# Kernel tuning notes

Measured on AMD Instinct MI355X. Metric: run time of the kernel, lower is better.

The kernel has to match this reference:

```python
import jax, jax.numpy as jnp
import numpy as np

TEMP = 0.07


def setup_inputs() -> dict:
    key = jax.random.key(0)
    k1, k2 = jax.random.split(key)
    N, C = 8192, 512
    X = jax.random.normal(k1, (N, C), dtype=jnp.float32)
    Y = jax.random.normal(k2, (N, C), dtype=jnp.float32)
    return {"X": X, "Y": Y}


def reference(X, Y):
    # Original loop computes, per row i, cross-entropy over logits
    # [X_i.Y_i, X_i.Y_j (j != i)] / temp with label 0 (the positive).
    # Softmax CE is permutation-invariant, so this equals
    #   logsumexp(S_i / temp) - S_ii / temp,  S = X @ Y^T,
    # summed over rows (loop accumulates with +=, i.e. sum reduction).
    S = jnp.einsum('nc,mc->nm', X, Y) / TEMP  # [N, N]
    lse = jax.nn.logsumexp(S, axis=1)          # [N]
    pos = jnp.diagonal(S)                      # [N]
    return jnp.sum(lse - pos)
```

## Files before the change

kernel.cpp:

```cpp
#include <hip/hip_runtime.h>
#include <stdint.h>

#define N 8192
#define C 512
#define BM 256
#define BN 128
#define BKF 128
#define NSPLIT 8
#define COLS_PER_SPLIT (N / NSPLIT)
#define CT (COLS_PER_SPLIT / BN)
#define GRID_GEMM ((N / BM) * NSPLIT)
#define INV_T 14.285714285714286f

typedef __attribute__((ext_vector_type(4)))  int   i32x4;
typedef __attribute__((ext_vector_type(8)))  int   i32x8;
typedef __attribute__((ext_vector_type(16))) float f32x16;

__global__ __launch_bounds__(256) void prep_kernel(const float* __restrict__ X,
                                                   const float* __restrict__ Y,
                                                   unsigned char* __restrict__ Xf8,
                                                   unsigned char* __restrict__ Yf8,
                                                   float* __restrict__ pos,
                                                   int* __restrict__ cnt,
                                                   float* __restrict__ out) {
  if (blockIdx.x == 0) {
    if (threadIdx.x < (N / BM)) cnt[threadIdx.x] = 0;
    if (threadIdx.x == 64) *out = 0.0f;
  }
  const int wave = threadIdx.x >> 6;
  const int lane = threadIdx.x & 63;
  const int row = blockIdx.x * 4 + wave;
  const float4* xr = (const float4*)(X + (size_t)row * C) + lane * 2;
  const float4* yr = (const float4*)(Y + (size_t)row * C) + lane * 2;
  float4 x0 = xr[0], x1 = xr[1];
  float4 y0 = yr[0], y1 = yr[1];
  float s = x0.x * y0.x + x0.y * y0.y + x0.z * y0.z + x0.w * y0.w
          + x1.x * y1.x + x1.y * y1.y + x1.z * y1.z + x1.w * y1.w;
  int2 ox, oy;
  ox.x = __builtin_amdgcn_cvt_pk_fp8_f32(x0.x, x0.y, 0, false);
  ox.x = __builtin_amdgcn_cvt_pk_fp8_f32(x0.z, x0.w, ox.x, true);
  ox.y = __builtin_amdgcn_cvt_pk_fp8_f32(x1.x, x1.y, 0, false);
  ox.y = __builtin_amdgcn_cvt_pk_fp8_f32(x1.z, x1.w, ox.y, true);
  oy.x = __builtin_amdgcn_cvt_pk_fp8_f32(y0.x, y0.y, 0, false);
  oy.x = __builtin_amdgcn_cvt_pk_fp8_f32(y0.z, y0.w, oy.x, true);
  oy.y = __builtin_amdgcn_cvt_pk_fp8_f32(y1.x, y1.y, 0, false);
  oy.y = __builtin_amdgcn_cvt_pk_fp8_f32(y1.z, y1.w, oy.y, true);
  ((int2*)(Xf8 + (size_t)row * C))[lane] = ox;
  ((int2*)(Yf8 + (size_t)row * C))[lane] = oy;
#pragma unroll
  for (int off = 32; off >= 1; off >>= 1) s += __shfl_xor(s, off);
  if (lane == 0) pos[row] = s * INV_T;
}

__global__ __launch_bounds__(256, 1) void gemm_lse_kernel(const unsigned char* __restrict__ Xf8,
                                                          const unsigned char* __restrict__ Yf8,
                                                          float2* __restrict__ partials,
                                                          const float* __restrict__ pos,
                                                          int* __restrict__ cnt,
                                                          float* __restrict__ out) {
  __shared__ unsigned char Bs[2][BN][BKF];
  __shared__ float wsum[4];
  __shared__ int mflag;

  const int tid = threadIdx.x;
  const int bx = blockIdx.x;
  const int split = bx & (NSPLIT - 1);
  const int rb = bx >> 3;
  const int row0 = rb * BM;
  const int colbase = split * COLS_PER_SPLIT;

  const int w = tid >> 6;
  const int lane = tid & 63;
  const int lrow = lane & 31;
  const int h = lane >> 5;
  const int swz = lrow & 7;

  i32x4 tL0[8], tH0[8], tL1[8], tH1[8];
  {
    const unsigned char* a0 = Xf8 + (size_t)(row0 + w * 64 + lrow) * C + h * 32;
    const unsigned char* a1 = a0 + (size_t)32 * C;
#pragma unroll
    for (int kk = 0; kk < 8; ++kk) {
      asm volatile("global_load_dwordx4 %0, %1, off"
                   : "=v"(tL0[kk]) : "v"(a0 + kk * 64));
      asm volatile("global_load_dwordx4 %0, %1, off offset:16"
                   : "=v"(tH0[kk]) : "v"(a0 + kk * 64));
      asm volatile("global_load_dwordx4 %0, %1, off"
                   : "=v"(tL1[kk]) : "v"(a1 + kk * 64));
      asm volatile("global_load_dwordx4 %0, %1, off offset:16"
                   : "=v"(tH1[kk]) : "v"(a1 + kk * 64));
    }
  }

  const int r_base = tid >> 3;
  const int p = tid & 7;
  const int j = p ^ (r_base & 7);

  auto stageB = [&](int buf, int col0, int k0) {
#pragma unroll
    for (int i = 0; i < 4; ++i) {
      const int r = i * 32 + r_base;
      const unsigned char* gb = Yf8 + (size_t)(col0 + r) * C + k0 * BKF + j * 16;
      uint32_t loff = (uint32_t)((i * 256 + (tid & ~63)) * 16);
      __builtin_amdgcn_global_load_lds(
          (const __attribute__((address_space(1))) uint32_t*)(uintptr_t)gb,
          (__attribute__((address_space(3))) uint32_t*)(uintptr_t)((char*)&Bs[buf][0][0] + loff),
          16, 0, 0);
    }
  };

  stageB(0, colbase, 0);
  asm volatile("s_waitcnt vmcnt(0)" ::: "memory");
  __builtin_amdgcn_sched_barrier(0);
  __builtin_amdgcn_s_barrier();
  __builtin_amdgcn_sched_barrier(0);

  i32x8 aF0[8], aF1[8];
#pragma unroll
  for (int kk = 0; kk < 8; ++kk) {
    aF0[kk] = (i32x8){ tL0[kk][0], tL0[kk][1], tL0[kk][2], tL0[kk][3],
                       tH0[kk][0], tH0[kk][1], tH0[kk][2], tH0[kk][3] };
    aF1[kk] = (i32x8){ tL1[kk][0], tL1[kk][1], tL1[kk][2], tL1[kk][3],
                       tH1[kk][0], tH1[kk][1], tH1[kk][2], tH1[kk][3] };
  }

  float m0[16], l0[16], m1[16], l1[16];
#pragma unroll
  for (int s = 0; s < 16; ++s) {
    m0[s] = -INFINITY; l0[s] = 0.0f;
    m1[s] = -INFINITY; l1[s] = 0.0f;
  }

  for (int ct = 0; ct < CT; ++ct) {
    f32x16 acc0[4], acc1[4];
#pragma unroll
    for (int t = 0; t < 4; ++t)
#pragma unroll
      for (int e = 0; e < 16; ++e) { acc0[t][e] = 0.0f; acc1[t][e] = 0.0f; }

#pragma unroll
    for (int k0 = 0; k0 < 4; ++k0) {
      const int nct = (k0 == 3) ? ((ct + 1) & (CT - 1)) : ct;
      const int nk0 = (k0 + 1) & 3;
      stageB((k0 + 1) & 1, colbase + nct * BN, nk0);
      __builtin_amdgcn_sched_barrier(0);
      asm volatile("s_waitcnt vmcnt(4)" ::: "memory");
      __builtin_amdgcn_s_barrier();
      __builtin_amdgcn_sched_barrier(0);

      __builtin_amdgcn_s_setprio(1);
#pragma unroll
      for (int s = 0; s < 2; ++s) {
        const int kk = 2 * k0 + s;
        const int c0 = 4 * s + 2 * h;
#pragma unroll
        for (int tj = 0; tj < 4; ++tj) {
          const int brow = tj * 32 + lrow;
          i32x4 blo = *(const i32x4*)&Bs[k0 & 1][brow][((c0    ) ^ swz) * 16];
          i32x4 bhi = *(const i32x4*)&Bs[k0 & 1][brow][((c0 + 1) ^ swz) * 16];
          i32x8 bf = { blo[0], blo[1], blo[2], blo[3], bhi[0], bhi[1], bhi[2], bhi[3] };
          acc0[tj] = __builtin_amdgcn_mfma_scale_f32_32x32x64_f8f6f4(
              aF0[kk], bf, acc0[tj], 0, 0, 0, 127, 0, 127);
          acc1[tj] = __builtin_amdgcn_mfma_scale_f32_32x32x64_f8f6f4(
              aF1[kk], bf, acc1[tj], 0, 0, 0, 127, 0, 127);
        }
      }
      __builtin_amdgcn_s_setprio(0);
      __builtin_amdgcn_sched_barrier(0);
      __builtin_amdgcn_s_barrier();
      __builtin_amdgcn_sched_barrier(0);
    }

#pragma unroll
    for (int r = 0; r < 16; ++r) {
      {
        float v0 = acc0[0][r] * INV_T, v1 = acc0[1][r] * INV_T;
        float v2 = acc0[2][r] * INV_T, v3 = acc0[3][r] * INV_T;
        float mx = fmaxf(fmaxf(v0, v1), fmaxf(v2, v3));
        float mn = fmaxf(m0[r], mx);
        l0[r] = l0[r] * __expf(m0[r] - mn)
              + __expf(v0 - mn) + __expf(v1 - mn) + __expf(v2 - mn) + __expf(v3 - mn);
        m0[r] = mn;
      }
      {
        float v0 = acc1[0][r] * INV_T, v1 = acc1[1][r] * INV_T;
        float v2 = acc1[2][r] * INV_T, v3 = acc1[3][r] * INV_T;
        float mx = fmaxf(fmaxf(v0, v1), fmaxf(v2, v3));
        float mn = fmaxf(m1[r], mx);
        l1[r] = l1[r] * __expf(m1[r] - mn)
              + __expf(v0 - mn) + __expf(v1 - mn) + __expf(v2 - mn) + __expf(v3 - mn);
        m1[r] = mn;
      }
    }
  }

  asm volatile("s_waitcnt vmcnt(0)" ::: "memory");

#pragma unroll
  for (int r = 0; r < 16; ++r) {
    float ma = m0[r], la = l0[r], mb = m1[r], lb = l1[r];
#pragma unroll
    for (int off = 1; off < 32; off <<= 1) {
      float mo = __shfl_xor(ma, off), lo = __shfl_xor(la, off);
      float mn = fmaxf(ma, mo);
      la = la * __expf(ma - mn) + lo * __expf(mo - mn);
      ma = mn;
      float mo2 = __shfl_xor(mb, off), lo2 = __shfl_xor(lb, off);
      float mn2 = fmaxf(mb, mo2);
      lb = lb * __expf(mb - mn2) + lo2 * __expf(mo2 - mn2);
      mb = mn2;
    }
    m0[r] = ma; l0[r] = la; m1[r] = mb; l1[r] = lb;
  }
  if (lrow == 0) {
#pragma unroll
    for (int r = 0; r < 16; ++r) {
      int row_local = (r & 3) + 8 * (r >> 2) + 4 * h;
      int base = row0 + w * 64;
      partials[(size_t)split * N + (base + row_local)]      = make_float2(m0[r], l0[r]);
      partials[(size_t)split * N + (base + 32 + row_local)] = make_float2(m1[r], l1[r]);
    }
  }

  __syncthreads();
  if (tid == 0) {
    __threadfence();
    int old = atomicAdd(&cnt[rb], 1);
    mflag = (old == NSPLIT - 1) ? 1 : 0;
  }
  __syncthreads();
  if (mflag) {
    __threadfence();
    int row = row0 + tid;
    float M = -INFINITY, L = 0.0f;
#pragma unroll
    for (int s = 0; s < NSPLIT; ++s) {
      float2 pr = partials[(size_t)s * N + row];
      float mn = fmaxf(M, pr.x);
      L = L * __expf(M - mn) + pr.y * __expf(pr.x - mn);
      M = mn;
    }
    float v = M + __logf(L) - pos[row];
#pragma unroll
    for (int off = 32; off >= 1; off >>= 1) v += __shfl_xor(v, off);
    if (lane == 0) wsum[w] = v;
    __syncthreads();
    if (tid == 0) atomicAdd(out, wsum[0] + wsum[1] + wsum[2] + wsum[3]);
  }
}

extern "C" void kernel_launch(void* const* d_in, const int* in_sizes, int n_in,
                              void* d_out, int out_size, void* d_ws, size_t ws_size,
                              hipStream_t stream) {
  const float* X = (const float*)d_in[0];
  const float* Y = (const float*)d_in[1];
  float* out = (float*)d_out;

  char* w = (char*)d_ws;
  unsigned char* Xf8 = (unsigned char*)w;
  unsigned char* Yf8 = Xf8 + (size_t)N * C;
  float2* partials = (float2*)(Yf8 + (size_t)N * C);
  float* pos = (float*)((char*)partials + (size_t)NSPLIT * N * sizeof(float2));
  int* cnt = (int*)(pos + N);

  prep_kernel<<<N / 4, 256, 0, stream>>>(X, Y, Xf8, Yf8, pos, cnt, out);
  gemm_lse_kernel<<<GRID_GEMM, 256, 0, stream>>>(Xf8, Yf8, partials, pos, cnt, out);
}
```

Measured before the change: 140.2 us.

## Shrink row tile to 64, split columns across waves, use exp2 online softmax

Reduces the GEMM row tile from 256 to 64 rows so each wave handles a 32-column slice of the B tile instead of all 128 columns. This quadruples the grid and allows two blocks per CU, targeting occupancy and per-wave register pressure. The cost is less A/B reuse per block: each staged B tile now feeds only 64 rows, so B traffic rises fourfold. The LSE update switches to base-2 exponentials with a prescaled factor, and a shared-memory cross-wave merge is added before partials are written.

```diff
diff --git a/kernel.cpp b/kernel.cpp
--- a/kernel.cpp
+++ b/kernel.cpp
@@ -3,14 +3,17 @@
 
 #define N 8192
 #define C 512
-#define BM 256
+#define BM 64
 #define BN 128
 #define BKF 128
 #define NSPLIT 8
 #define COLS_PER_SPLIT (N / NSPLIT)
 #define CT (COLS_PER_SPLIT / BN)
-#define GRID_GEMM ((N / BM) * NSPLIT)
+#define NRB (N / BM)
+#define GRID_GEMM (NRB * NSPLIT)
 #define INV_T 14.285714285714286f
+#define SCALE2 20.60992915555662f
+#define LN2F 0.6931471805599453f
 
 typedef __attribute__((ext_vector_type(4)))  int   i32x4;
 typedef __attribute__((ext_vector_type(8)))  int   i32x8;
@@ -24,8 +27,8 @@
                                                    int* __restrict__ cnt,
                                                    float* __restrict__ out) {
   if (blockIdx.x == 0) {
-    if (threadIdx.x < (N / BM)) cnt[threadIdx.x] = 0;
-    if (threadIdx.x == 64) *out = 0.0f;
+    if (threadIdx.x < NRB) cnt[threadIdx.x] = 0;
+    if (threadIdx.x == 128) *out = 0.0f;
   }
   const int wave = threadIdx.x >> 6;
   const int lane = threadIdx.x & 63;
@@ -52,7 +55,7 @@
   if (lane == 0) pos[row] = s * INV_T;
 }
 
-__global__ __launch_bounds__(256, 1) void gemm_lse_kernel(const unsigned char* __restrict__ Xf8,
+__global__ __launch_bounds__(256, 2) void gemm_lse_kernel(const unsigned char* __restrict__ Xf8,
                                                           const unsigned char* __restrict__ Yf8,
                                                           float2* __restrict__ partials,
                                                           const float* __restrict__ pos,
@@ -74,21 +77,15 @@
   const int lrow = lane & 31;
   const int h = lane >> 5;
   const int swz = lrow & 7;
-
-  i32x4 tL0[8], tH0[8], tL1[8], tH1[8];
+  const int brow = w * 32 + lrow;
+
+  i32x8 aF0[8], aF1[8];
   {
-    const unsigned char* a0 = Xf8 + (size_t)(row0 + w * 64 + lrow) * C + h * 32;
-    const unsigned char* a1 = a0 + (size_t)32 * C;
+    const unsigned char* a0 = Xf8 + (size_t)(row0 + lrow) * C + h * 32;
 #pragma unroll
     for (int kk = 0; kk < 8; ++kk) {
-      asm volatile("global_load_dwordx4 %0, %1, off"
-                   : "=v"(tL0[kk]) : "v"(a0 + kk * 64));
-      asm volatile("global_load_dwordx4 %0, %1, off offset:16"
-                   : "=v"(tH0[kk]) : "v"(a0 + kk * 64));
-      asm volatile("global_load_dwordx4 %0, %1, off"
-                   : "=v"(tL1[kk]) : "v"(a1 + kk * 64));
-      asm volatile("global_load_dwordx4 %0, %1, off offset:16"
-                   : "=v"(tH1[kk]) : "v"(a1 + kk * 64));
+      aF0[kk] = *(const i32x8*)(a0 + kk * 64);
+      aF1[kk] = *(const i32x8*)(a0 + (size_t)32 * C + kk * 64);
     }
   }
 
@@ -110,19 +107,8 @@
   };
 
   stageB(0, colbase, 0);
-  asm volatile("s_waitcnt vmcnt(0)" ::: "memory");
+  __syncthreads();
   __builtin_amdgcn_sched_barrier(0);
-  __builtin_amdgcn_s_barrier();
-  __builtin_amdgcn_sched_barrier(0);
-
-  i32x8 aF0[8], aF1[8];
-#pragma unroll
-  for (int kk = 0; kk < 8; ++kk) {
-    aF0[kk] = (i32x8){ tL0[kk][0], tL0[kk][1], tL0[kk][2], tL0[kk][3],
-                       tH0[kk][0], tH0[kk][1], tH0[kk][2], tH0[kk][3] };
-    aF1[kk] = (i32x8){ tL1[kk][0], tL1[kk][1], tL1[kk][2], tL1[kk][3],
-                       tH1[kk][0], tH1[kk][1], tH1[kk][2], tH1[kk][3] };
-  }
 
   float m0[16], l0[16], m1[16], l1[16];
 #pragma unroll
@@ -132,11 +118,9 @@
   }
 
   for (int ct = 0; ct < CT; ++ct) {
-    f32x16 acc0[4], acc1[4];
-#pragma unroll
-    for (int t = 0; t < 4; ++t)
-#pragma unroll
-      for (int e = 0; e < 16; ++e) { acc0[t][e] = 0.0f; acc1[t][e] = 0.0f; }
+    f32x16 acc0, acc1;
+#pragma unroll
+    for (int e = 0; e < 16; ++e) { acc0[e] = 0.0f; acc1[e] = 0.0f; }
 
 #pragma unroll
     for (int k0 = 0; k0 < 4; ++k0) {
@@ -149,21 +133,18 @@
       __builtin_amdgcn_sched_barrier(0);
 
       __builtin_amdgcn_s_setprio(1);
+      const unsigned char* bbase = &Bs[k0 & 1][brow][0];
 #pragma unroll
       for (int s = 0; s < 2; ++s) {
         const int kk = 2 * k0 + s;
         const int c0 = 4 * s + 2 * h;
-#pragma unroll
-        for (int tj = 0; tj < 4; ++tj) {
-          const int brow = tj * 32 + lrow;
-          i32x4 blo = *(const i32x4*)&Bs[k0 & 1][brow][((c0    ) ^ swz) * 16];
-          i32x4 bhi = *(const i32x4*)&Bs[k0 & 1][brow][((c0 + 1) ^ swz) * 16];
-          i32x8 bf = { blo[0], blo[1], blo[2], blo[3], bhi[0], bhi[1], bhi[2], bhi[3] };
-          acc0[tj] = __builtin_amdgcn_mfma_scale_f32_32x32x64_f8f6f4(
-              aF0[kk], bf, acc0[tj], 0, 0, 0, 127, 0, 127);
-          acc1[tj] = __builtin_amdgcn_mfma_scale_f32_32x32x64_f8f6f4(
-              aF1[kk], bf, acc1[tj], 0, 0, 0, 127, 0, 127);
-        }
+        i32x8 bf;
+        *(i32x4*)&bf         = *(const i32x4*)(bbase + ((c0    ) ^ swz) * 16);
+        *(((i32x4*)&bf) + 1) = *(const i32x4*)(bbase + ((c0 + 1) ^ swz) * 16);
+        acc0 = __builtin_amdgcn_mfma_scale_f32_32x32x64_f8f6f4(
+            aF0[kk], bf, acc0, 0, 0, 0, 127, 0, 127);
+        acc1 = __builtin_amdgcn_mfma_scale_f32_32x32x64_f8f6f4(
+            aF1[kk], bf, acc1, 0, 0, 0, 127, 0, 127);
       }
       __builtin_amdgcn_s_setprio(0);
       __builtin_amdgcn_sched_barrier(0);
@@ -173,24 +154,14 @@
 
 #pragma unroll
     for (int r = 0; r < 16; ++r) {
-      {
-        float v0 = acc0[0][r] * INV_T, v1 = acc0[1][r] * INV_T;
-        float v2 = acc0[2][r] * INV_T, v3 = acc0[3][r] * INV_T;
-        float mx = fmaxf(fmaxf(v0, v1), fmaxf(v2, v3));
-        float mn = fmaxf(m0[r], mx);
-        l0[r] = l0[r] * __expf(m0[r] - mn)
-              + __expf(v0 - mn) + __expf(v1 - mn) + __expf(v2 - mn) + __expf(v3 - mn);
-        m0[r] = mn;
-      }
-      {
-        float v0 = acc1[0][r] * INV_T, v1 = acc1[1][r] * INV_T;
-        float v2 = acc1[2][r] * INV_T, v3 = acc1[3][r] * INV_T;
-        float mx = fmaxf(fmaxf(v0, v1), fmaxf(v2, v3));
-        float mn = fmaxf(m1[r], mx);
-        l1[r] = l1[r] * __expf(m1[r] - mn)
-              + __expf(v0 - mn) + __expf(v1 - mn) + __expf(v2 - mn) + __expf(v3 - mn);
-        m1[r] = mn;
-      }
+      float u0 = acc0[r] * SCALE2;
+      float n0 = fmaxf(m0[r], u0);
+      l0[r] = l0[r] * exp2f(m0[r] - n0) + exp2f(u0 - n0);
+      m0[r] = n0;
+      float u1 = acc1[r] * SCALE2;
+      float n1 = fmaxf(m1[r], u1);
+      l1[r] = l1[r] * exp2f(m1[r] - n1) + exp2f(u1 - n1);
+      m1[r] = n1;
     }
   }
 
@@ -203,23 +174,40 @@
     for (int off = 1; off < 32; off <<= 1) {
       float mo = __shfl_xor(ma, off), lo = __shfl_xor(la, off);
       float mn = fmaxf(ma, mo);
-      la = la * __expf(ma - mn) + lo * __expf(mo - mn);
+      la = la * exp2f(ma - mn) + lo * exp2f(mo - mn);
       ma = mn;
       float mo2 = __shfl_xor(mb, off), lo2 = __shfl_xor(lb, off);
       float mn2 = fmaxf(mb, mo2);
-      lb = lb * __expf(mb - mn2) + lo2 * __expf(mo2 - mn2);
+      lb = lb * exp2f(mb - mn2) + lo2 * exp2f(mo2 - mn2);
       mb = mn2;
     }
     m0[r] = ma; l0[r] = la; m1[r] = mb; l1[r] = lb;
   }
+
+  __syncthreads();
+  float2* mb2 = (float2*)&Bs[0][0][0];
   if (lrow == 0) {
 #pragma unroll
     for (int r = 0; r < 16; ++r) {
-      int row_local = (r & 3) + 8 * (r >> 2) + 4 * h;
-      int base = row0 + w * 64;
-      partials[(size_t)split * N + (base + row_local)]      = make_float2(m0[r], l0[r]);
-      partials[(size_t)split * N + (base + 32 + row_local)] = make_float2(m1[r], l1[r]);
-    }
+      mb2[((w * 2 + 0) * 2 + h) * 16 + r] = make_float2(m0[r], l0[r]);
+      mb2[((w * 2 + 1) * 2 + h) * 16 + r] = make_float2(m1[r], l1[r]);
+    }
+  }
+  __syncthreads();
+  if (tid < BM) {
+    const int ar = tid >> 5;
+    const int rl = tid & 31;
+    const int hI = (rl >> 2) & 1;
+    const int rI = (rl & 3) + 4 * (rl >> 3);
+    float M = -INFINITY, L = 0.0f;
+#pragma unroll
+    for (int wcI = 0; wcI < 4; ++wcI) {
+      float2 pr = mb2[((wcI * 2 + ar) * 2 + hI) * 16 + rI];
+      float mn = fmaxf(M, pr.x);
+      L = L * exp2f(M - mn) + pr.y * exp2f(pr.x - mn);
+      M = mn;
+    }
+    partials[(size_t)split * N + (row0 + tid)] = make_float2(M, L);
   }
 
   __syncthreads();
@@ -231,16 +219,19 @@
   __syncthreads();
   if (mflag) {
     __threadfence();
-    int row = row0 + tid;
-    float M = -INFINITY, L = 0.0f;
-#pragma unroll
-    for (int s = 0; s < NSPLIT; ++s) {
-      float2 pr = partials[(size_t)s * N + row];
-      float mn = fmaxf(M, pr.x);
-      L = L * __expf(M - mn) + pr.y * __expf(pr.x - mn);
-      M = mn;
-    }
-    float v = M + __logf(L) - pos[row];
+    float v = 0.0f;
+    if (tid < BM) {
+      const int row = row0 + tid;
+      float M = -INFINITY, L = 0.0f;
+#pragma unroll
+      for (int s = 0; s < NSPLIT; ++s) {
+        float2 pr = partials[(size_t)s * N + row];
+        float mn = fmaxf(M, pr.x);
+        L = L * exp2f(M - mn) + pr.y * exp2f(pr.x - mn);
+        M = mn;
+      }
+      v = LN2F * (M + log2f(L)) - pos[row];
+    }
 #pragma unroll
     for (int off = 32; off >= 1; off >>= 1) v += __shfl_xor(v, off);
     if (lane == 0) wsum[w] = v;
```

Measured after the change: 244.6 us. 74.5% more time.
